# Kernel optimization log

Measured on AMD Instinct MI355X. Metric: run time of the kernel, lower is better.

## Reference

```python
import jax, jax.numpy as jnp
import numpy as np

D, DK, DV, H = 1024, 64, 1024, 16
DVH = DV // H  # per-head value dim
EPS = 1e-5


def _layer_norm(x, g, b):
    mu = jnp.mean(x, axis=-1, keepdims=True)
    var = jnp.var(x, axis=-1, keepdims=True)
    return (x - mu) * jax.lax.rsqrt(var + EPS) * g + b


def setup_inputs() -> dict:
    key = jax.random.key(0)
    ks = jax.random.split(key, 12)
    s = lambda k, shape, fan_in: jax.random.normal(k, shape, jnp.float32) / np.sqrt(fan_in)
    return {
        "x": jax.random.normal(ks[0], (2, 2048, D), jnp.float32),
        "Wq": s(ks[1], (H, D, DK), D),
        "Wk": s(ks[2], (H, D, DK), D),
        "Wv": s(ks[3], (H, D, DVH), D),
        "Wo": s(ks[4], (DV, D), DV),
        "ln1_g": jnp.ones((D,), jnp.float32),
        "ln1_b": jnp.zeros((D,), jnp.float32),
        "W1": s(ks[5], (D, 4 * D), D),
        "b1": jnp.zeros((4 * D,), jnp.float32),
        "W2": s(ks[6], (4 * D, D), 4 * D),
        "b2": jnp.zeros((D,), jnp.float32),
        "ln2_g": jnp.ones((D,), jnp.float32),
        "ln2_b": jnp.zeros((D,), jnp.float32),
    }


def reference(x, Wq, Wk, Wv, Wo, ln1_g, ln1_b, W1, b1, W2, b2, ln2_g, ln2_b):
    B, S, _ = x.shape
    # per-head projections (vectorized over the head loop of the original)
    q = jnp.einsum("bsd,hdk->bhsk", x, Wq)
    k = jnp.einsum("bsd,hdk->bhsk", x, Wk)
    v = jnp.einsum("bsd,hdv->bhsv", x, Wv)
    scores = jnp.einsum("bhsk,bhtk->bhst", q, k) / np.sqrt(DK).astype(np.float32)
    attn = jax.nn.softmax(scores, axis=-1)
    o = jnp.einsum("bhst,bhtv->bhsv", attn, v)  # [B,H,S,DVH]
    o = o.transpose(0, 2, 1, 3).reshape(B, S, DV)  # concat heads
    attn_out = o @ Wo
    x1 = _layer_norm(attn_out + x, ln1_g, ln1_b)
    ffn = jax.nn.relu(x1 @ W1 + b1) @ W2 + b2
    return _layer_norm(ffn + x1, ln2_g, ln2_b)
```

## Files before the change

### kernel.cpp

```cpp
#include <hip/hip_runtime.h>
#include <hip/hip_bf16.h>

typedef unsigned short u16;
typedef unsigned int u32;
typedef short short8 __attribute__((ext_vector_type(8)));
typedef float fx4 __attribute__((ext_vector_type(4)));
typedef u32 ux4 __attribute__((ext_vector_type(4)));
typedef u32 ux2 __attribute__((ext_vector_type(2)));

__device__ __forceinline__ float b2f(u16 x) {
  return __uint_as_float(((u32)x) << 16);
}
__device__ __forceinline__ u16 f2b(float f) {
  u32 u = __float_as_uint(f);
  u += 0x7fffu + ((u >> 16) & 1u);
  return (u16)(u >> 16);
}
__device__ __forceinline__ u32 cvtpk(float a, float b) {
  u32 r;
  asm("v_cvt_pk_bf16_f32 %0, %1, %2" : "=v"(r) : "v"(a), "v"(b));
  return r;
}

__device__ __forceinline__ void load16(const u16* g, u16* l) {
  __builtin_amdgcn_global_load_lds(
      (__attribute__((address_space(1))) void*)(u16*)g,
      (__attribute__((address_space(3))) void*)l, 16, 0, 0);
}

__global__ __launch_bounds__(256) void cvt_f2b_kernel(
    const float* __restrict__ in, u16* __restrict__ out)
{
  int i = (blockIdx.x * 256 + threadIdx.x) * 4;
  fx4 v = *(const fx4*)(in + i);
  u16 o4[4];
#pragma unroll
  for (int j = 0; j < 4; ++j) o4[j] = f2b(v[j]);
  *(uint2*)(out + i) = *(uint2*)o4;
}

__global__ __launch_bounds__(256) void transpose_f2b_kernel(
    const float* __restrict__ in, u16* __restrict__ out,
    int R, int C, int out_ld)
{
  __shared__ __align__(16) u16 tile[32][33];
  int tx = threadIdx.x, ty = threadIdx.y;
  int c0 = blockIdx.x * 32, r0 = blockIdx.y * 32;
  const float* inb = in + (size_t)blockIdx.z * R * C;
  u16* outb = out + (size_t)blockIdx.z * C * out_ld;
#pragma unroll
  for (int i = 0; i < 4; ++i)
    tile[ty + i * 8][tx] = f2b(inb[(size_t)(r0 + ty + i * 8) * C + c0 + tx]);
  __syncthreads();
#pragma unroll
  for (int i = 0; i < 4; ++i)
    outb[(size_t)(c0 + ty + i * 8) * out_ld + r0 + tx] = tile[tx][ty + i * 8];
}

__global__ __launch_bounds__(256) void transpose_b2b_kernel(
    const u16* __restrict__ in, u16* __restrict__ out, int in_ld, int out_ld)
{
  __shared__ __align__(16) u16 tile[32][33];
  int tx = threadIdx.x, ty = threadIdx.y;
  int c0 = blockIdx.x * 32, r0 = blockIdx.y * 32;
#pragma unroll
  for (int i = 0; i < 4; ++i)
    tile[ty + i * 8][tx] = in[(size_t)(r0 + ty + i * 8) * in_ld + c0 + tx];
  __syncthreads();
#pragma unroll
  for (int i = 0; i < 4; ++i)
    out[(size_t)(c0 + ty + i * 8) * out_ld + r0 + tx] = tile[tx][ty + i * 8];
}

__global__ __launch_bounds__(256, 2) void gemm_bt(
    const u16* __restrict__ A, const u16* __restrict__ BT,
    const float* __restrict__ bias, void* __restrict__ Cp,
    int M, int N, int K, int flags)
{
  __shared__ __align__(16) u16 As[2][4096];
  __shared__ __align__(16) u16 Bs[2][4096];
  int tid = threadIdx.x;
  int lane = tid & 63, wid = tid >> 6;
  int l15 = lane & 15, quad = lane >> 4;
  int wm = wid >> 1, wn = wid & 1;
  int m0 = blockIdx.y * 128, n0 = blockIdx.x * 128;

  int srow = wid * 16 + (lane >> 2);
  int sswz = (((lane >> 2) & 3) + ((lane >> 4) & 3)) & 3;
  int gch = (lane & 3) ^ sswz;
  const u16* gA = A + (size_t)(m0 + srow) * K + gch * 8;
  const u16* gB = BT + (size_t)(n0 + srow) * K + gch * 8;
  size_t gstep = (size_t)64 * K;
  u16* lA = &As[0][wid * 512];
  u16* lB = &Bs[0][wid * 512];

  int rswz = ((l15 & 3) + (l15 >> 2)) & 3;
  int rphys = ((quad ^ rswz) & 3) << 3;

  fx4 acc[4][4];
#pragma unroll
  for (int i = 0; i < 4; ++i)
#pragma unroll
    for (int j = 0; j < 4; ++j) acc[i][j] = fx4{0.f, 0.f, 0.f, 0.f};

  int nt = K >> 5;
  load16(gA,         lA);
  load16(gA + gstep, lA + 2048);
  load16(gB,         lB);
  load16(gB + gstep, lB + 2048);

  for (int kt = 0; kt < nt; ++kt) {
    __syncthreads();
    if (kt + 1 < nt) {
      int buf = (kt + 1) & 1;
      const u16* ga = gA + (kt + 1) * 32;
      const u16* gb = gB + (kt + 1) * 32;
      load16(ga,         lA + buf * 4096);
      load16(ga + gstep, lA + buf * 4096 + 2048);
      load16(gb,         lB + buf * 4096);
      load16(gb + gstep, lB + buf * 4096 + 2048);
    }
    const u16* Ab = As[kt & 1];
    const u16* Bb = Bs[kt & 1];
    short8 af[4], bf[4];
#pragma unroll
    for (int t = 0; t < 4; ++t)
      af[t] = *(const short8*)&Ab[(wm * 64 + t * 16 + l15) * 32 + rphys];
#pragma unroll
    for (int t = 0; t < 4; ++t)
      bf[t] = *(const short8*)&Bb[(wn * 64 + t * 16 + l15) * 32 + rphys];
#pragma unroll
    for (int tm = 0; tm < 4; ++tm)
#pragma unroll
      for (int tn = 0; tn < 4; ++tn)
        acc[tm][tn] = __builtin_amdgcn_mfma_f32_16x16x32_bf16(
            af[tm], bf[tn], acc[tm][tn], 0, 0, 0);
  }

  bool obf = flags & 1, hb = flags & 2, rl = flags & 4;
#pragma unroll
  for (int tn = 0; tn < 4; ++tn) {
    int col = n0 + wn * 64 + tn * 16 + l15;
    float bv = hb ? bias[col] : 0.0f;
#pragma unroll
    for (int tm = 0; tm < 4; ++tm) {
      int row = m0 + wm * 64 + tm * 16 + (quad << 2);
#pragma unroll
      for (int r = 0; r < 4; ++r) {
        float v = acc[tm][tn][r] + bv;
        if (rl) v = fmaxf(v, 0.0f);
        size_t idx = (size_t)(row + r) * N + col;
        if (obf) ((u16*)Cp)[idx] = f2b(v);
        else ((float*)Cp)[idx] = v;
      }
    }
  }
}

__global__ __launch_bounds__(256, 2) void gemm_bt_k64(
    const u16* __restrict__ A, const u16* __restrict__ BT,
    const float* __restrict__ bias, void* __restrict__ Cp,
    int M, int N, int K, int flags)
{
  __shared__ __align__(16) u16 As[2][8192];
  __shared__ __align__(16) u16 Bs[2][8192];
  int tid = threadIdx.x;
  int lane = tid & 63, wid = tid >> 6;
  int l15 = lane & 15, quad = lane >> 4;
  int wm = wid >> 1, wn = wid & 1;

  int bx = blockIdx.x, by = blockIdx.y, bz = blockIdx.z;
  if (gridDim.z > 1) {
    int nx = gridDim.x, ny = gridDim.y;
    int total = nx * ny * (int)gridDim.z;
    int cpx = total >> 3;
    int lin = bx + nx * (by + ny * bz);
    int swb = (lin & 7) * cpx + (lin >> 3);
    bx = swb % nx;
    int t2 = swb / nx;
    by = t2 % ny;
    bz = t2 / ny;
  }
  int m0 = by * 128, n0 = bx * 128;
  int kc = K / (int)gridDim.z;

  int r8 = lane >> 3;
  int clog = (lane & 7) ^ r8;
  const u16* gA = A + (size_t)(m0 + wid * 8 + r8) * K + bz * kc + clog * 8;
  const u16* gB = BT + (size_t)(n0 + wid * 8 + r8) * K + bz * kc + clog * 8;
  size_t gstep = (size_t)32 * K;
  u16* lA = &As[0][wid * 512];
  u16* lB = &Bs[0][wid * 512];

  fx4 acc[4][4];
#pragma unroll
  for (int i = 0; i < 4; ++i)
#pragma unroll
    for (int j = 0; j < 4; ++j) acc[i][j] = fx4{0.f, 0.f, 0.f, 0.f};

  int nt = kc >> 6;
#pragma unroll
  for (int i = 0; i < 4; ++i) {
    load16(gA + i * gstep, lA + i * 2048);
    load16(gB + i * gstep, lB + i * 2048);
  }

  for (int kt = 0; kt < nt; ++kt) {
    __syncthreads();
    if (kt + 1 < nt) {
      int buf = (kt + 1) & 1;
      const u16* ga = gA + (kt + 1) * 64;
      const u16* gb = gB + (kt + 1) * 64;
#pragma unroll
      for (int i = 0; i < 4; ++i) {
        load16(ga + i * gstep, lA + buf * 8192 + i * 2048);
        load16(gb + i * gstep, lB + buf * 8192 + i * 2048);
      }
    }
    const u16* Ab = As[kt & 1];
    const u16* Bb = Bs[kt & 1];
#pragma unroll
    for (int s = 0; s < 2; ++s) {
      int ch = (((s << 2) | quad) ^ (l15 & 7)) << 3;
      short8 af[4], bf[4];
#pragma unroll
      for (int t = 0; t < 4; ++t)
        af[t] = *(const short8*)&Ab[(wm * 64 + t * 16 + l15) * 64 + ch];
#pragma unroll
      for (int t = 0; t < 4; ++t)
        bf[t] = *(const short8*)&Bb[(wn * 64 + t * 16 + l15) * 64 + ch];
#pragma unroll
      for (int tm = 0; tm < 4; ++tm)
#pragma unroll
        for (int tn = 0; tn < 4; ++tn)
          acc[tm][tn] = __builtin_amdgcn_mfma_f32_16x16x32_bf16(
              af[tm], bf[tn], acc[tm][tn], 0, 0, 0);
    }
  }

  bool obf = flags & 1, hb = flags & 2, rl = flags & 4;
  u16* cb16 = (u16*)Cp + (size_t)bz * M * N;
  float* cf32 = (float*)Cp + (size_t)bz * M * N;
#pragma unroll
  for (int tn = 0; tn < 4; ++tn) {
    int col = n0 + wn * 64 + tn * 16 + l15;
    float bv = hb ? bias[col] : 0.0f;
#pragma unroll
    for (int tm = 0; tm < 4; ++tm) {
      int row = m0 + wm * 64 + tm * 16 + (quad << 2);
#pragma unroll
      for (int r = 0; r < 4; ++r) {
        float v = acc[tm][tn][r] + bv;
        if (rl) v = fmaxf(v, 0.0f);
        size_t idx = (size_t)(row + r) * N + col;
        if (obf) cb16[idx] = f2b(v);
        else cf32[idx] = v;
      }
    }
  }
}

__global__ __launch_bounds__(256, 2) void attn_kernel(
    const u16* __restrict__ qkv, const u16* __restrict__ vT,
    u16* __restrict__ o)
{
  __shared__ __align__(16) u16 Ks[2][4096];
  __shared__ __align__(16) u16 Vs[2][4096];
  int tid = threadIdx.x;
  int lane = tid & 63, wid = tid >> 6;
  int l15 = lane & 15, quad = lane >> 4;
  int b = blockIdx.z, h = blockIdx.y;
  int q0 = blockIdx.x * 128 + wid * 32;

  const u16* qbA = qkv + (size_t)(b * 2048 + q0 + l15) * 3072 + h * 64 + (quad << 3);
  short8 qA0 = *(const short8*)qbA;
  short8 qA1 = *(const short8*)(qbA + 32);
  const u16* qbB = qbA + (size_t)16 * 3072;
  short8 qB0 = *(const short8*)qbB;
  short8 qB1 = *(const short8*)(qbB + 32);

  int srow = tid >> 3;
  int gc8 = ((tid & 7) ^ (srow & 7)) << 3;
  const u16* kg = qkv + (size_t)(b * 2048 + srow) * 3072 + 1024 + h * 64 + gc8;
  const u16* vg = vT + (size_t)(h * 64 + srow) * 4096 + b * 2048 + gc8;
  u16* lk = &Ks[0][wid * 512];
  u16* lv = &Vs[0][wid * 512];

  int lq = l15 >> 2;
  int rs = ((((lq & 1) << 1) | (lq >> 1)) << 2) | (l15 & 3);
  int sk = rs & 7;

  fx4 oaccA[4], oaccB[4];
  float sumA = 0.0f, sumB = 0.0f;
#pragma unroll
  for (int i = 0; i < 4; ++i) {
    oaccA[i] = fx4{0.f, 0.f, 0.f, 0.f};
    oaccB[i] = fx4{0.f, 0.f, 0.f, 0.f};
  }

  load16(kg,             lk);
  load16(kg + 32 * 3072, lk + 2048);
  load16(vg,             lv);
  load16(vg + 32 * 4096, lv + 2048);

  int swz = l15 & 7;
  const float SC = 0.18033688011112042f;
  for (int kt = 0; kt < 32; ++kt) {
    __syncthreads();
    if (kt + 1 < 32) {
      int buf = (kt + 1) & 1;
      const u16* kgn = kg + (size_t)(kt + 1) * 64 * 3072;
      const u16* vgn = vg + (kt + 1) * 64;
      load16(kgn,             lk + buf * 4096);
      load16(kgn + 32 * 3072, lk + buf * 4096 + 2048);
      load16(vgn,             lv + buf * 4096);
      load16(vgn + 32 * 4096, lv + buf * 4096 + 2048);
    }
    const u16* Kb = Ks[kt & 1];
    const u16* Vb = Vs[kt & 1];

    fx4 scA[4], scB[4];
    __builtin_amdgcn_s_setprio(1);
#pragma unroll
    for (int sub = 0; sub < 4; ++sub) {
      const u16* rp = &Kb[(sub * 16 + rs) * 64];
      short8 kf0 = *(const short8*)&rp[((quad ^ sk) & 7) << 3];
      short8 kf1 = *(const short8*)&rp[(((4 | quad) ^ sk) & 7) << 3];
      scA[sub] = fx4{0.f, 0.f, 0.f, 0.f};
      scA[sub] = __builtin_amdgcn_mfma_f32_16x16x32_bf16(kf0, qA0, scA[sub], 0, 0, 0);
      scA[sub] = __builtin_amdgcn_mfma_f32_16x16x32_bf16(kf1, qA1, scA[sub], 0, 0, 0);
      scB[sub] = fx4{0.f, 0.f, 0.f, 0.f};
      scB[sub] = __builtin_amdgcn_mfma_f32_16x16x32_bf16(kf0, qB0, scB[sub], 0, 0, 0);
      scB[sub] = __builtin_amdgcn_mfma_f32_16x16x32_bf16(kf1, qB1, scB[sub], 0, 0, 0);
    }
    __builtin_amdgcn_s_setprio(0);

    u32 WA[4][2], WB[4][2];
    float psA = 0.0f, psB = 0.0f;
#pragma unroll
    for (int sub = 0; sub < 4; ++sub) {
      float a0 = __builtin_amdgcn_exp2f(scA[sub][0] * SC);
      float a1 = __builtin_amdgcn_exp2f(scA[sub][1] * SC);
      float a2 = __builtin_amdgcn_exp2f(scA[sub][2] * SC);
      float a3 = __builtin_amdgcn_exp2f(scA[sub][3] * SC);
      psA += (a0 + a1) + (a2 + a3);
      WA[sub][0] = cvtpk(a0, a1);
      WA[sub][1] = cvtpk(a2, a3);
      float b0 = __builtin_amdgcn_exp2f(scB[sub][0] * SC);
      float b1 = __builtin_amdgcn_exp2f(scB[sub][1] * SC);
      float b2 = __builtin_amdgcn_exp2f(scB[sub][2] * SC);
      float b3 = __builtin_amdgcn_exp2f(scB[sub][3] * SC);
      psB += (b0 + b1) + (b2 + b3);
      WB[sub][0] = cvtpk(b0, b1);
      WB[sub][1] = cvtpk(b2, b3);
    }
    sumA += psA;
    sumB += psB;

    ux2 eA00 = __builtin_amdgcn_permlane32_swap(WA[0][0], WA[1][0], false, false);
    ux2 eA01 = __builtin_amdgcn_permlane32_swap(WA[0][1], WA[1][1], false, false);
    ux2 eA10 = __builtin_amdgcn_permlane32_swap(WA[2][0], WA[3][0], false, false);
    ux2 eA11 = __builtin_amdgcn_permlane32_swap(WA[2][1], WA[3][1], false, false);
    short8 pa1A = __builtin_bit_cast(short8, ux4{eA00[0], eA01[0], eA00[1], eA01[1]});
    short8 pa2A = __builtin_bit_cast(short8, ux4{eA10[0], eA11[0], eA10[1], eA11[1]});
    ux2 eB00 = __builtin_amdgcn_permlane32_swap(WB[0][0], WB[1][0], false, false);
    ux2 eB01 = __builtin_amdgcn_permlane32_swap(WB[0][1], WB[1][1], false, false);
    ux2 eB10 = __builtin_amdgcn_permlane32_swap(WB[2][0], WB[3][0], false, false);
    ux2 eB11 = __builtin_amdgcn_permlane32_swap(WB[2][1], WB[3][1], false, false);
    short8 pa1B = __builtin_bit_cast(short8, ux4{eB00[0], eB01[0], eB00[1], eB01[1]});
    short8 pa2B = __builtin_bit_cast(short8, ux4{eB10[0], eB11[0], eB10[1], eB11[1]});

    __builtin_amdgcn_s_setprio(1);
#pragma unroll
    for (int dt = 0; dt < 4; ++dt) {
      const u16* rp = &Vb[(dt * 16 + l15) * 64];
      short8 vf0 = *(const short8*)&rp[((quad ^ swz) & 7) << 3];
      short8 vf1 = *(const short8*)&rp[(((4 | quad) ^ swz) & 7) << 3];
      oaccA[dt] = __builtin_amdgcn_mfma_f32_16x16x32_bf16(pa1A, vf0, oaccA[dt], 0, 0, 0);
      oaccA[dt] = __builtin_amdgcn_mfma_f32_16x16x32_bf16(pa2A, vf1, oaccA[dt], 0, 0, 0);
      oaccB[dt] = __builtin_amdgcn_mfma_f32_16x16x32_bf16(pa1B, vf0, oaccB[dt], 0, 0, 0);
      oaccB[dt] = __builtin_amdgcn_mfma_f32_16x16x32_bf16(pa2B, vf1, oaccB[dt], 0, 0, 0);
    }
    __builtin_amdgcn_s_setprio(0);
  }
  sumA += __shfl_xor(sumA, 16, 64);
  sumA += __shfl_xor(sumA, 32, 64);
  sumB += __shfl_xor(sumB, 16, 64);
  sumB += __shfl_xor(sumB, 32, 64);
  fx4 invA, invB;
#pragma unroll
  for (int r = 0; r < 4; ++r) {
    invA[r] = 1.0f / __shfl(sumA, (quad << 2) + r, 64);
    invB[r] = 1.0f / __shfl(sumB, (quad << 2) + r, 64);
  }
#pragma unroll
  for (int dt = 0; dt < 4; ++dt) {
    int col = h * 64 + dt * 16 + l15;
#pragma unroll
    for (int r = 0; r < 4; ++r) {
      size_t rowA = (size_t)(b * 2048 + q0 + (quad << 2) + r);
      o[rowA * 1024 + col] = f2b(oaccA[dt][r] * invA[r]);
      o[(rowA + 16) * 1024 + col] = f2b(oaccB[dt][r] * invB[r]);
    }
  }
}

__global__ __launch_bounds__(256) void ln_kernel(
    const float* __restrict__ main0, const float* __restrict__ main1,
    const float* __restrict__ res, const float* __restrict__ cbias,
    const float* __restrict__ g, const float* __restrict__ beta,
    u16* __restrict__ out_b, float* __restrict__ out_f)
{
  __shared__ float red[8];
  int row = blockIdx.x, tid = threadIdx.x;
  size_t base = (size_t)row * 1024 + tid * 4;
  fx4 v = *(const fx4*)(main0 + base);
  fx4 v1 = *(const fx4*)(main1 + base);
  fx4 rv = *(const fx4*)(res + base);
#pragma unroll
  for (int i = 0; i < 4; ++i) v[i] += v1[i] + rv[i];
  if (cbias) {
    fx4 cb = *(const fx4*)(cbias + tid * 4);
#pragma unroll
    for (int i = 0; i < 4; ++i) v[i] += cb[i];
  }
  float s = v[0] + v[1] + v[2] + v[3];
  float sq = v[0] * v[0] + v[1] * v[1] + v[2] * v[2] + v[3] * v[3];
#pragma unroll
  for (int off = 32; off >= 1; off >>= 1) {
    s += __shfl_xor(s, off, 64);
    sq += __shfl_xor(sq, off, 64);
  }
  int wid = tid >> 6, lane = tid & 63;
  if (lane == 0) { red[wid] = s; red[wid + 4] = sq; }
  __syncthreads();
  float S = red[0] + red[1] + red[2] + red[3];
  float SQ = red[4] + red[5] + red[6] + red[7];
  float mean = S * (1.0f / 1024.0f);
  float var = SQ * (1.0f / 1024.0f) - mean * mean;
  float rs = rsqrtf(var + 1e-5f);
  fx4 gv = *(const fx4*)(g + tid * 4);
  fx4 bv = *(const fx4*)(beta + tid * 4);
  float of[4];
#pragma unroll
  for (int i = 0; i < 4; ++i) of[i] = (v[i] - mean) * rs * gv[i] + bv[i];
  if (out_f) *(fx4*)(out_f + base) = *(const fx4*)of;
  if (out_b) {
    u16 o4[4];
#pragma unroll
    for (int i = 0; i < 4; ++i) o4[i] = f2b(of[i]);
    *(uint2*)(out_b + base) = *(uint2*)o4;
  }
}

extern "C" void kernel_launch(void* const* d_in, const int* in_sizes, int n_in,
                              void* d_out, int out_size, void* d_ws, size_t ws_size,
                              hipStream_t stream) {
  (void)in_sizes; (void)n_in; (void)out_size; (void)ws_size;
  const float* x     = (const float*)d_in[0];
  const float* Wq    = (const float*)d_in[1];
  const float* Wk    = (const float*)d_in[2];
  const float* Wv    = (const float*)d_in[3];
  const float* Wo    = (const float*)d_in[4];
  const float* g1    = (const float*)d_in[5];
  const float* bb1   = (const float*)d_in[6];
  const float* W1    = (const float*)d_in[7];
  const float* bias1 = (const float*)d_in[8];
  const float* W2    = (const float*)d_in[9];
  const float* bias2 = (const float*)d_in[10];
  const float* g2    = (const float*)d_in[11];
  const float* bb2   = (const float*)d_in[12];

  char* ws = (char*)d_ws;
  const size_t MB = 1048576;
  u16* xb     = (u16*)(ws);
  u16* wqkvT  = (u16*)(ws + 8 * MB);
  u16* woT    = (u16*)(ws + 38 * MB);
  u16* qkv    = (u16*)(ws + 40 * MB);
  u16* vT     = (u16*)(ws + 64 * MB);
  u16* ob     = (u16*)(ws + 72 * MB);
  float* aout = (float*)(ws);
  u16* x1     = (u16*)(ws + 64 * MB);
  float* x1f  = (float*)(ws + 40 * MB);
  u16* w1T    = (u16*)(ws + 56 * MB);
  u16* w2T    = (u16*)(ws);
  u16* hbuf   = (u16*)(ws + 8 * MB);
  float* ffn  = (float*)(ws + 56 * MB);

  dim3 tb(32, 8, 1);
  cvt_f2b_kernel<<<4096, 256, 0, stream>>>(x, xb);
  transpose_f2b_kernel<<<dim3(2, 32, 16), tb, 0, stream>>>(Wq, wqkvT,           1024, 64, 1024);
  transpose_f2b_kernel<<<dim3(2, 32, 16), tb, 0, stream>>>(Wk, wqkvT + 1048576, 1024, 64, 1024);
  transpose_f2b_kernel<<<dim3(2, 32, 16), tb, 0, stream>>>(Wv, wqkvT + 2097152, 1024, 64, 1024);
  transpose_f2b_kernel<<<dim3(32, 32, 1), tb, 0, stream>>>(Wo, woT, 1024, 1024, 1024);

  gemm_bt<<<dim3(24, 32), 256, 0, stream>>>(xb, wqkvT, nullptr, qkv, 4096, 3072, 1024, 1);
  transpose_b2b_kernel<<<dim3(32, 128), tb, 0, stream>>>(qkv + 2048, vT, 3072, 4096);
  attn_kernel<<<dim3(16, 16, 2), 256, 0, stream>>>(qkv, vT, ob);
  gemm_bt_k64<<<dim3(8, 32, 2), 256, 0, stream>>>(ob, woT, nullptr, aout, 4096, 1024, 1024, 0);
  ln_kernel<<<4096, 256, 0, stream>>>(aout, aout + 4194304, x, nullptr, g1, bb1, x1, x1f);
  transpose_f2b_kernel<<<dim3(128, 32, 1), tb, 0, stream>>>(W1, w1T, 1024, 4096, 1024);
  transpose_f2b_kernel<<<dim3(32, 128, 1), tb, 0, stream>>>(W2, w2T, 4096, 1024, 4096);
  gemm_bt<<<dim3(32, 32), 256, 0, stream>>>(x1, w1T, bias1, hbuf, 4096, 4096, 1024, 1 | 2 | 4);
  gemm_bt_k64<<<dim3(8, 32, 2), 256, 0, stream>>>(hbuf, w2T, nullptr, ffn, 4096, 1024, 4096, 0);
  ln_kernel<<<4096, 256, 0, stream>>>(ffn, ffn + 4194304, x1f, bias2, g2, bb2, nullptr, (float*)d_out);
}
```

Baseline: 352.1 us.

## Split attention key range in two and combine partial outputs in a separate kernel

The attention kernel now splits the 2048-key range into two halves, which doubles the grid. Each block writes unnormalized fp32 partial outputs and per-row softmax denominators to workspace. A new combine kernel adds the two partials, normalizes them and writes the bf16 head outputs. The aim is more parallel blocks and shorter per-block loops. The cost is extra fp32 global traffic for the partials and one more kernel launch.

```diff
diff --git a/kernel.cpp b/kernel.cpp
--- a/kernel.cpp
+++ b/kernel.cpp
@@ -262,15 +262,18 @@
 
 __global__ __launch_bounds__(256, 2) void attn_kernel(
     const u16* __restrict__ qkv, const u16* __restrict__ vT,
-    u16* __restrict__ o)
+    float* __restrict__ po, float* __restrict__ ps)
 {
   __shared__ __align__(16) u16 Ks[2][4096];
   __shared__ __align__(16) u16 Vs[2][4096];
   int tid = threadIdx.x;
   int lane = tid & 63, wid = tid >> 6;
   int l15 = lane & 15, quad = lane >> 4;
-  int b = blockIdx.z, h = blockIdx.y;
+  int bz = blockIdx.z;
+  int b = bz >> 1, half = bz & 1;
+  int h = blockIdx.y;
   int q0 = blockIdx.x * 128 + wid * 32;
+  int k0 = half * 1024;
 
   const u16* qbA = qkv + (size_t)(b * 2048 + q0 + l15) * 3072 + h * 64 + (quad << 3);
   short8 qA0 = *(const short8*)qbA;
@@ -281,8 +284,8 @@
 
   int srow = tid >> 3;
   int gc8 = ((tid & 7) ^ (srow & 7)) << 3;
-  const u16* kg = qkv + (size_t)(b * 2048 + srow) * 3072 + 1024 + h * 64 + gc8;
-  const u16* vg = vT + (size_t)(h * 64 + srow) * 4096 + b * 2048 + gc8;
+  const u16* kg = qkv + (size_t)(b * 2048 + k0 + srow) * 3072 + 1024 + h * 64 + gc8;
+  const u16* vg = vT + (size_t)(h * 64 + srow) * 4096 + b * 2048 + k0 + gc8;
   u16* lk = &Ks[0][wid * 512];
   u16* lv = &Vs[0][wid * 512];
 
@@ -305,9 +308,9 @@
 
   int swz = l15 & 7;
   const float SC = 0.18033688011112042f;
-  for (int kt = 0; kt < 32; ++kt) {
+  for (int kt = 0; kt < 16; ++kt) {
     __syncthreads();
-    if (kt + 1 < 32) {
+    if (kt + 1 < 16) {
       int buf = (kt + 1) & 1;
       const u16* kgn = kg + (size_t)(kt + 1) * 64 * 3072;
       const u16* vgn = vg + (kt + 1) * 64;
@@ -387,22 +390,39 @@
   sumA += __shfl_xor(sumA, 32, 64);
   sumB += __shfl_xor(sumB, 16, 64);
   sumB += __shfl_xor(sumB, 32, 64);
-  fx4 invA, invB;
-#pragma unroll
-  for (int r = 0; r < 4; ++r) {
-    invA[r] = 1.0f / __shfl(sumA, (quad << 2) + r, 64);
-    invB[r] = 1.0f / __shfl(sumB, (quad << 2) + r, 64);
-  }
+  if (lane < 16) {
+    size_t rowA = (size_t)(b * 2048 + q0 + lane);
+    ps[(rowA * 16 + h) * 2 + half] = sumA;
+    ps[((rowA + 16) * 16 + h) * 2 + half] = sumB;
+  }
+  float* pob = po + (size_t)half * 4194304;
 #pragma unroll
   for (int dt = 0; dt < 4; ++dt) {
     int col = h * 64 + dt * 16 + l15;
 #pragma unroll
     for (int r = 0; r < 4; ++r) {
       size_t rowA = (size_t)(b * 2048 + q0 + (quad << 2) + r);
-      o[rowA * 1024 + col] = f2b(oaccA[dt][r] * invA[r]);
-      o[(rowA + 16) * 1024 + col] = f2b(oaccB[dt][r] * invB[r]);
-    }
-  }
+      pob[rowA * 1024 + col] = oaccA[dt][r];
+      pob[(rowA + 16) * 1024 + col] = oaccB[dt][r];
+    }
+  }
+}
+
+__global__ __launch_bounds__(256) void attn_combine_kernel(
+    const float* __restrict__ po, const float* __restrict__ ps,
+    u16* __restrict__ o)
+{
+  int row = blockIdx.x, tid = threadIdx.x;
+  size_t base = (size_t)row * 1024 + tid * 4;
+  fx4 a = *(const fx4*)(po + base);
+  fx4 c = *(const fx4*)(po + 4194304 + base);
+  int h = (tid * 4) >> 6;
+  const float* pr = ps + ((size_t)row * 16 + h) * 2;
+  float inv = 1.0f / (pr[0] + pr[1]);
+  u16 o4[4];
+#pragma unroll
+  for (int i = 0; i < 4; ++i) o4[i] = f2b((a[i] + c[i]) * inv);
+  *(uint2*)(o + base) = *(uint2*)o4;
 }
 
 __global__ __launch_bounds__(256) void ln_kernel(
@@ -479,6 +499,8 @@
   u16* qkv    = (u16*)(ws + 40 * MB);
   u16* vT     = (u16*)(ws + 64 * MB);
   u16* ob     = (u16*)(ws + 72 * MB);
+  float* po   = (float*)(ws);
+  float* ps   = (float*)(ws + 32 * MB);
   float* aout = (float*)(ws);
   u16* x1     = (u16*)(ws + 64 * MB);
   float* x1f  = (float*)(ws + 40 * MB);
@@ -496,7 +518,8 @@
 
   gemm_bt<<<dim3(24, 32), 256, 0, stream>>>(xb, wqkvT, nullptr, qkv, 4096, 3072, 1024, 1);
   transpose_b2b_kernel<<<dim3(32, 128), tb, 0, stream>>>(qkv + 2048, vT, 3072, 4096);
-  attn_kernel<<<dim3(16, 16, 2), 256, 0, stream>>>(qkv, vT, ob);
+  attn_kernel<<<dim3(16, 16, 4), 256, 0, stream>>>(qkv, vT, po, ps);
+  attn_combine_kernel<<<4096, 256, 0, stream>>>(po, ps, ob);
   gemm_bt_k64<<<dim3(8, 32, 2), 256, 0, stream>>>(ob, woT, nullptr, aout, 4096, 1024, 1024, 0);
   ln_kernel<<<4096, 256, 0, stream>>>(aout, aout + 4194304, x, nullptr, g1, bb1, x1, x1f);
   transpose_f2b_kernel<<<dim3(128, 32, 1), tb, 0, stream>>>(W1, w1T, 1024, 4096, 1024);
```

After: 363.3 us. +3.2%, slower.
